# Optimization experiments

Hardware: AMD Instinct MI355X
Metric: run time of the kernel (lower is better)

## Reference

```python
import jax, jax.numpy as jnp
import numpy as np

EMB = 128
EDGE = 32
STEPS = 3


def _lrelu(x):
    return jax.nn.leaky_relu(x, negative_slope=0.01)


def setup_inputs() -> dict:
    key = jax.random.key(0)
    ks = jax.random.split(key, 16)
    N, E, G = 50000, 400000, 256
    x = jax.random.normal(ks[0], (N, EMB), jnp.float32)
    edge_attr = jax.random.normal(ks[1], (E, EDGE), jnp.float32)
    edge_index = jax.random.randint(ks[2], (2, E), 0, N, jnp.int64)
    batch_ind = jnp.sort(jax.random.randint(ks[3], (N,), 0, G, jnp.int64))
    data_lens = jax.random.randint(ks[4], (G,), 0, G, jnp.int64)
    s = 1.0 / np.sqrt(EMB)
    Wm = jax.random.normal(ks[5], (STEPS, EMB + EDGE, EMB), jnp.float32) * s
    bm = jnp.zeros((STEPS, EMB), jnp.float32)
    Wa = jax.random.normal(ks[6], (STEPS, 3 * EMB, EMB), jnp.float32) * s
    ba = jnp.zeros((STEPS, EMB), jnp.float32)
    Wgate = jax.random.normal(ks[7], (STEPS, EMB), jnp.float32) * s
    bgate = jnp.zeros((STEPS,), jnp.float32)
    Wfeat = jax.random.normal(ks[8], (STEPS, EMB, EMB), jnp.float32) * s
    bfeat = jnp.zeros((STEPS, EMB), jnp.float32)
    Wt = jax.random.normal(ks[9], (STEPS, 2 * EMB, EMB), jnp.float32) * s
    bt = jnp.zeros((STEPS, EMB), jnp.float32)
    return {"x": x, "edge_attr": edge_attr, "Wm": Wm, "bm": bm, "Wa": Wa,
            "ba": ba, "Wgate": Wgate, "bgate": bgate, "Wfeat": Wfeat,
            "bfeat": bfeat, "Wt": Wt, "bt": bt, "edge_index": edge_index,
            "batch_ind": batch_ind, "num_graphs": 256, "data_lens": data_lens}


def reference(x, edge_attr, Wm, bm, Wa, ba, Wgate, bgate, Wfeat, bfeat, Wt, bt,
              edge_index, batch_ind, num_graphs, data_lens):
    N = x.shape[0]
    src, dst = edge_index[0], edge_index[1]  # PyG: x_j = x[src], aggregate at dst
    xg = jnp.zeros((num_graphs, EMB), x.dtype)  # xg_init is None -> zeros
    for s in range(STEPS):
        # GraphNet: gather -> message MLP -> scatter-max -> update MLP + residual
        xg_node = xg[batch_ind]                                   # [N, emb]
        z = jnp.concatenate([x[src], edge_attr], axis=1)          # [E, emb+edge]
        m = _lrelu(z @ Wm[s] + bm[s])                             # [E, emb]
        agg = jax.ops.segment_max(m, dst, num_segments=N)         # [N, emb]
        agg = jnp.where(jnp.isneginf(agg), 0.0, agg)              # PyG fills empty with 0
        z2 = jnp.concatenate([x, xg_node, agg], axis=1)           # [N, 3*emb]
        x = _lrelu(z2 @ Wa[s] + ba[s]) + x
        # GlobalNode: segment-softmax attention pooling + transform + residual
        gate = x @ Wgate[s] + bgate[s]                            # [N]
        gmax = jax.ops.segment_max(gate, batch_ind, num_segments=num_graphs)
        gmax = jnp.where(jnp.isneginf(gmax), 0.0, gmax)
        e = jnp.exp(gate - gmax[batch_ind])
        denom = jax.ops.segment_sum(e, batch_ind, num_segments=num_graphs)
        alpha = e / denom[batch_ind]                              # [N]
        feat = _lrelu(x @ Wfeat[s] + bfeat[s])                    # [N, emb]
        pooled = jax.ops.segment_sum(alpha[:, None] * feat, batch_ind,
                                     num_segments=num_graphs)     # [G, emb]
        cat = jnp.concatenate([pooled, xg], axis=1)               # [G, 2*emb]
        xg = _lrelu(cat @ Wt[s] + bt[s]) + xg
    return x, xg
```

## Files before the change

kernel.cpp:

```cpp
#include <hip/hip_runtime.h>
#include <hip/hip_bf16.h>

#define EMB 128
#define EDGE 32
#define STEPS 3

typedef short bf8s __attribute__((ext_vector_type(8)));
typedef float f32x4 __attribute__((ext_vector_type(4)));

__device__ __forceinline__ float lrelu(float v) { return v > 0.0f ? v : 0.01f * v; }
__device__ __forceinline__ unsigned short f2bf(float f) {
    unsigned u = __float_as_uint(f);
    u += 0x7fffu + ((u >> 16) & 1u);
    return (unsigned short)(u >> 16);
}
__device__ __forceinline__ float bf2f(unsigned short s) {
    return __uint_as_float(((unsigned)s) << 16);
}
__device__ __forceinline__ unsigned pk2bf(float x, float y) {
    __hip_bfloat162 h = __float22bfloat162_rn(make_float2(x, y));
    return *(unsigned*)&h;
}

__global__ void k_hist(const int* __restrict__ dst, int E, int* __restrict__ deg) {
    int e = blockIdx.x * 256 + threadIdx.x;
    if (e < E) atomicAdd(&deg[dst[e]], 1);
}

__global__ void k_scan1(const int* __restrict__ deg, int N, int* __restrict__ rowptr,
                        int* __restrict__ bsums) {
    __shared__ int s[256];
    int t = threadIdx.x;
    int i = blockIdx.x * 256 + t;
    int v = (i < N) ? deg[i] : 0;
    s[t] = v;
    __syncthreads();
#pragma unroll
    for (int off = 1; off < 256; off <<= 1) {
        int x = (t >= off) ? s[t - off] : 0;
        __syncthreads();
        s[t] += x;
        __syncthreads();
    }
    if (i < N) rowptr[i] = s[t] - v;
    if (t == 255) bsums[blockIdx.x] = s[255];
}

__global__ void k_scan2(int* __restrict__ bsums, int NB) {
    __shared__ int s[256];
    __shared__ int carry;
    int t = threadIdx.x;
    if (t == 0) carry = 0;
    __syncthreads();
    for (int base = 0; base < NB; base += 256) {
        int i = base + t;
        int v = (i < NB) ? bsums[i] : 0;
        s[t] = v;
        __syncthreads();
#pragma unroll
        for (int off = 1; off < 256; off <<= 1) {
            int x = (t >= off) ? s[t - off] : 0;
            __syncthreads();
            s[t] += x;
            __syncthreads();
        }
        int excl = s[t] - v + carry;
        if (i < NB) bsums[i] = excl;
        int tot = s[255];
        __syncthreads();
        if (t == 0) carry += tot;
        __syncthreads();
    }
}

__global__ void k_scan3(int* __restrict__ rowptr, const int* __restrict__ bsums,
                        int* __restrict__ cursor, int N, int E) {
    int i = blockIdx.x * 256 + threadIdx.x;
    if (i < N) {
        int v = rowptr[i] + bsums[i >> 8];
        rowptr[i] = v;
        cursor[i] = v;
    }
    if (i == 0) rowptr[N] = E;
}

__global__ void k_fill(const int* __restrict__ src, const int* __restrict__ dst, int E,
                       int* __restrict__ cursor, int2* __restrict__ sp2) {
    int e = blockIdx.x * 256 + threadIdx.x;
    if (e >= E) return;
    int d = dst[e];
    int p = atomicAdd(&cursor[d], 1);
    sp2[p] = make_int2(src[e], e);
}

__global__ __launch_bounds__(256) void k_eaperm(const float* __restrict__ ea,
                                                const int2* __restrict__ sp2,
                                                unsigned short* __restrict__ ea16p,
                                                int* __restrict__ srcp, int E) {
    int p = blockIdx.x * 256 + threadIdx.x;
    if (p >= E) return;
    int2 sp = sp2[p];
    srcp[p] = sp.x;
    const float4* er = (const float4*)(ea + (size_t)sp.y * EDGE);
    union { unsigned u[16]; int4 v[4]; } o;
#pragma unroll
    for (int q = 0; q < 8; ++q) {
        float4 v = er[q];
        o.u[2 * q]     = pk2bf(v.x, v.y);
        o.u[2 * q + 1] = pk2bf(v.z, v.w);
    }
    int4* dp = (int4*)(ea16p + (size_t)p * EDGE);
#pragma unroll
    for (int q = 0; q < 4; ++q) dp[q] = o.v[q];
}

__global__ __launch_bounds__(256) void k_setup(const float* __restrict__ x0,
                                               unsigned short* __restrict__ x16,
                                               int N, int XB, int NB,
                                               const float* __restrict__ ba,
                                               float* __restrict__ gb,
                                               float* __restrict__ xg_a,
                                               const int* __restrict__ batch,
                                               int* __restrict__ gstart, int G,
                                               unsigned short* __restrict__ h16,
                                               int* __restrict__ deg) {
    int b = blockIdx.x, t = threadIdx.x;
    if (b < XB) {
        size_t idx = ((size_t)b * 256 + t) * 8;
        if (idx < (size_t)N * EMB) {
            const float4* s = (const float4*)(x0 + idx);
            float4 v0 = s[0], v1 = s[1];
            union { bf8s v; unsigned u[4]; } o;
            o.u[0] = pk2bf(v0.x, v0.y);
            o.u[1] = pk2bf(v0.z, v0.w);
            o.u[2] = pk2bf(v1.x, v1.y);
            o.u[3] = pk2bf(v1.z, v1.w);
            *(bf8s*)(x16 + idx) = o.v;
        }
        return;
    }
    b -= XB;
    if (b < NB) {
        int i = b * 256 + t;
        if (i < N) deg[i] = 0;
        return;
    }
    b -= NB;
    if (b < G) {
        if (t < EMB) gb[(size_t)b * EMB + t] = ba[t];
        else xg_a[(size_t)b * EMB + (t - EMB)] = 0.f;
        if (t == 0) {
            int lo = 0, hi = N;
            while (lo < hi) {
                int mid = (lo + hi) >> 1;
                if (batch[mid] < b) lo = mid + 1; else hi = mid;
            }
            gstart[b] = lo;
        }
        return;
    }
    if (t < EMB) h16[(size_t)N * EMB + t] = 0xFF80u;
    if (t == EMB) gstart[G] = N;
}

__global__ __launch_bounds__(256) void k_wpack(const float* __restrict__ Wm,
                                               const float* __restrict__ Wa,
                                               const float* __restrict__ Wfeat,
                                               unsigned short* __restrict__ wpack) {
    int gid = blockIdx.x * 256 + threadIdx.x;
    int unit = gid >> 14;
    int e = gid & 16383;
    int s = unit / 5, u = unit % 5;
    const float* src; int rows;
    switch (u) {
        case 0: src = Wm + (size_t)s * 160 * EMB;             rows = 128; break;
        case 1: src = Wm + (size_t)s * 160 * EMB + 128 * EMB; rows = 32;  break;
        case 2: src = Wa + (size_t)s * 384 * EMB;             rows = 128; break;
        case 3: src = Wa + (size_t)s * 384 * EMB + 256 * EMB; rows = 128; break;
        default: src = Wfeat + (size_t)s * EMB * EMB;         rows = 128; break;
    }
    int k = e >> 7, n = e & 127;
    if (k >= rows) return;
    unsigned short b = f2bf(src[(size_t)k * EMB + n]);
    int kc = k >> 5, c = n >> 4, lane = (n & 15) | (((k & 31) >> 3) << 4), j = k & 7;
    wpack[(size_t)unit * 16384 + ((size_t)(kc * 8 + c) * 64 + lane) * 8 + j] = b;
}

__device__ __forceinline__ void loadAa(const unsigned short* __restrict__ A16, int row0,
                                       int wv, int lane, int N, bf8s af[4]) {
    int li = lane & 15, oct = lane >> 4;
    int m = row0 + wv * 16 + li;
    if (m >= N) m = N - 1;
    const bf8s* ar = (const bf8s*)(A16 + (size_t)m * EMB);
#pragma unroll
    for (int kc = 0; kc < 4; ++kc) af[kc] = ar[kc * 4 + oct];
}
__device__ __forceinline__ void stageB(const unsigned short* __restrict__ Bp,
                                       unsigned short* lB, int tid) {
#pragma unroll
    for (int i = 0; i < 8; ++i) {
        int idx = tid + i * 256;
        ((int4*)lB)[idx] = ((const int4*)Bp)[idx];
    }
}
__device__ __forceinline__ void mfma128r(const bf8s af[4], const unsigned short* lB,
                                         f32x4 acc[8], int lane) {
#pragma unroll
    for (int kc = 0; kc < 4; ++kc) {
#pragma unroll
        for (int c = 0; c < 8; ++c) {
            bf8s b = *(const bf8s*)&lB[((kc * 8 + c) * 64 + lane) * 8];
            acc[c] = __builtin_amdgcn_mfma_f32_16x16x32_bf16(af[kc], b, acc[c], 0, 0, 0);
        }
    }
}

__device__ __forceinline__ void bias_epi(const f32x4 acc[8], int row0, int wv, int lane,
                                         const float* __restrict__ bias,
                                         unsigned short* __restrict__ C, int N) {
    int li = lane & 15, quad = lane >> 4;
    float bcol[8];
#pragma unroll
    for (int c = 0; c < 8; ++c) bcol[c] = bias[c * 16 + li];
#pragma unroll
    for (int rr = 0; rr < 4; ++rr) {
        int m = row0 + wv * 16 + quad * 4 + rr;
        if (m < N) {
            union { bf8s v; unsigned u[4]; } o;
#pragma unroll
            for (int j = 0; j < 4; ++j)
                o.u[j] = pk2bf(acc[2 * j][rr] + bcol[2 * j],
                               acc[2 * j + 1][rr] + bcol[2 * j + 1]);
            *(bf8s*)&C[(size_t)m * EMB + li * 8] = o.v;
        }
    }
}

__global__ __launch_bounds__(256) void k_gemm_bias(const unsigned short* __restrict__ A16,
                                                   const unsigned short* __restrict__ Bp,
                                                   const float* __restrict__ bias,
                                                   unsigned short* __restrict__ C, int N) {
    __shared__ unsigned short lB[16384];
    int tid = threadIdx.x, wv = tid >> 6, lane = tid & 63;
    int row0 = blockIdx.x * 64;
    stageB(Bp, lB, tid);
    bf8s af[4];
    loadAa(A16, row0, wv, lane, N, af);
    __syncthreads();
    f32x4 acc[8];
#pragma unroll
    for (int c = 0; c < 8; ++c) acc[c] = (f32x4){0.f, 0.f, 0.f, 0.f};
    mfma128r(af, lB, acc, lane);
    bias_epi(acc, row0, wv, lane, bias, C, N);
}

__global__ __launch_bounds__(256) void k_gemm_node(unsigned short* __restrict__ x16,
                                                   const unsigned short* __restrict__ agg16,
                                                   const unsigned short* __restrict__ BpX,
                                                   const unsigned short* __restrict__ BpA,
                                                   const float* __restrict__ gb,
                                                   const int* __restrict__ batch,
                                                   float* __restrict__ xout_f32,
                                                   const float* __restrict__ wg,
                                                   const float* __restrict__ bg,
                                                   float* __restrict__ gate, int N) {
    __shared__ unsigned short lB[16384];
    int tid = threadIdx.x, wv = tid >> 6, lane = tid & 63;
    int row0 = blockIdx.x * 64;
    stageB(BpX, lB, tid);
    bf8s af[4];
    loadAa(x16, row0, wv, lane, N, af);
    __syncthreads();
    f32x4 acc[8];
#pragma unroll
    for (int c = 0; c < 8; ++c) acc[c] = (f32x4){0.f, 0.f, 0.f, 0.f};
    mfma128r(af, lB, acc, lane);
    __syncthreads();
    stageB(BpA, lB, tid);
    loadAa(agg16, row0, wv, lane, N, af);
    __syncthreads();
    mfma128r(af, lB, acc, lane);
    int li = lane & 15, quad = lane >> 4;
    float gpart[4] = {0.f, 0.f, 0.f, 0.f};
#pragma unroll
    for (int c = 0; c < 8; ++c) {
        int col = c * 16 + li;
        float wgc = wg[col];
#pragma unroll
        for (int rr = 0; rr < 4; ++rr) {
            int m = row0 + wv * 16 + quad * 4 + rr;
            if (m < N) {
                int g = batch[m];
                float b = gb[(size_t)g * EMB + col];
                float res = bf2f(x16[(size_t)m * EMB + col]);
                float v = lrelu(acc[c][rr] + b) + res;
                x16[(size_t)m * EMB + col] = f2bf(v);
                if (xout_f32) xout_f32[(size_t)m * EMB + col] = v;
                gpart[rr] = fmaf(v, wgc, gpart[rr]);
            }
        }
    }
#pragma unroll
    for (int rr = 0; rr < 4; ++rr) {
#pragma unroll
        for (int off = 1; off < 16; off <<= 1)
            gpart[rr] += __shfl_xor(gpart[rr], off, 64);
    }
    if (li == 0) {
        float b0 = bg[0];
#pragma unroll
        for (int rr = 0; rr < 4; ++rr) {
            int m = row0 + wv * 16 + quad * 4 + rr;
            if (m < N) gate[m] = gpart[rr] + b0;
        }
    }
}

__device__ __forceinline__ void feat_epi(const f32x4 acc[8], int row0, int wv, int lane,
                                         const float* __restrict__ bias,
                                         const float* __restrict__ gate,
                                         const float* __restrict__ gmax,
                                         const float* __restrict__ denom,
                                         const int* __restrict__ batch,
                                         float* __restrict__ pooled, int N) {
    int li = lane & 15, quad = lane >> 4;
    int rb = row0 + wv * 16;
    if (rb >= N) return;
    float alpha[4];
    int grow[4];
#pragma unroll
    for (int rr = 0; rr < 4; ++rr) {
        int m = rb + quad * 4 + rr;
        if (m < N) {
            int g = batch[m];
            grow[rr] = g;
            alpha[rr] = __expf(gate[m] - gmax[g]) / denom[g];
        } else { alpha[rr] = 0.f; grow[rr] = 0; }
    }
    int gs = batch[rb];
    int mlast = rb + 15; if (mlast >= N) mlast = N - 1;
    bool uni = (gs == batch[mlast]);
#pragma unroll
    for (int c = 0; c < 8; ++c) {
        int col = c * 16 + li;
        float b = bias[col];
        float v0 = alpha[0] * lrelu(acc[c][0] + b);
        float v1 = alpha[1] * lrelu(acc[c][1] + b);
        float v2 = alpha[2] * lrelu(acc[c][2] + b);
        float v3 = alpha[3] * lrelu(acc[c][3] + b);
        if (uni) {
            float s = (v0 + v1) + (v2 + v3);
            s += __shfl_xor(s, 16, 64);
            s += __shfl_xor(s, 32, 64);
            if (quad == 0) atomicAdd(&pooled[(size_t)gs * EMB + col], s);
        } else {
            if (rb + quad * 4 + 0 < N) atomicAdd(&pooled[(size_t)grow[0] * EMB + col], v0);
            if (rb + quad * 4 + 1 < N) atomicAdd(&pooled[(size_t)grow[1] * EMB + col], v1);
            if (rb + quad * 4 + 2 < N) atomicAdd(&pooled[(size_t)grow[2] * EMB + col], v2);
            if (rb + quad * 4 + 3 < N) atomicAdd(&pooled[(size_t)grow[3] * EMB + col], v3);
        }
    }
}

__global__ __launch_bounds__(256) void k_gemm_feat(const unsigned short* __restrict__ A16,
                                                   const unsigned short* __restrict__ Bp,
                                                   const float* __restrict__ bias,
                                                   const float* __restrict__ gate,
                                                   const float* __restrict__ gmax,
                                                   const float* __restrict__ denom,
                                                   const int* __restrict__ batch,
                                                   float* __restrict__ pooled, int N) {
    __shared__ unsigned short lB[16384];
    int tid = threadIdx.x, wv = tid >> 6, lane = tid & 63;
    int row0 = blockIdx.x * 64;
    stageB(Bp, lB, tid);
    bf8s af[4];
    loadAa(A16, row0, wv, lane, N, af);
    __syncthreads();
    f32x4 acc[8];
#pragma unroll
    for (int c = 0; c < 8; ++c) acc[c] = (f32x4){0.f, 0.f, 0.f, 0.f};
    mfma128r(af, lB, acc, lane);
    feat_epi(acc, row0, wv, lane, bias, gate, gmax, denom, batch, pooled, N);
}

__global__ __launch_bounds__(256) void k_gemm_fb(const unsigned short* __restrict__ A16,
                                                 const unsigned short* __restrict__ BpF,
                                                 const float* __restrict__ bfeat_s,
                                                 const float* __restrict__ gate,
                                                 const float* __restrict__ gmax,
                                                 const float* __restrict__ denom,
                                                 const int* __restrict__ batch,
                                                 float* __restrict__ pooled,
                                                 const unsigned short* __restrict__ BpBn,
                                                 const float* __restrict__ bm_next,
                                                 unsigned short* __restrict__ h16, int N) {
    __shared__ unsigned short lB[16384];
    int tid = threadIdx.x, wv = tid >> 6, lane = tid & 63;
    int row0 = blockIdx.x * 64;
    stageB(BpF, lB, tid);
    bf8s af[4];
    loadAa(A16, row0, wv, lane, N, af);
    __syncthreads();
    f32x4 accF[8], accB[8];
#pragma unroll
    for (int c = 0; c < 8; ++c) {
        accF[c] = (f32x4){0.f, 0.f, 0.f, 0.f};
        accB[c] = (f32x4){0.f, 0.f, 0.f, 0.f};
    }
    mfma128r(af, lB, accF, lane);
    __syncthreads();
    stageB(BpBn, lB, tid);
    __syncthreads();
    mfma128r(af, lB, accB, lane);
    feat_epi(accF, row0, wv, lane, bfeat_s, gate, gmax, denom, batch, pooled, N);
    bias_epi(accB, row0, wv, lane, bm_next, h16, N);
}

__global__ __launch_bounds__(256) void k_gseg(const float* __restrict__ gate,
                                              const int* __restrict__ gstart,
                                              float* __restrict__ gmax,
                                              float* __restrict__ denom,
                                              float* __restrict__ pooled) {
    int g = blockIdx.x;
    int t = threadIdx.x;
    if (t < EMB) pooled[(size_t)g * EMB + t] = 0.f;
    int s0 = gstart[g], s1 = gstart[g + 1];
    __shared__ float red[256];
    float mx = -__builtin_inff();
    for (int i = s0 + t; i < s1; i += 256) mx = fmaxf(mx, gate[i]);
    red[t] = mx;
    __syncthreads();
#pragma unroll
    for (int off = 128; off; off >>= 1) {
        if (t < off) red[t] = fmaxf(red[t], red[t + off]);
        __syncthreads();
    }
    float m = red[0];
    __syncthreads();
    float sum = 0.f;
    for (int i = s0 + t; i < s1; i += 256) sum += __expf(gate[i] - m);
    red[t] = sum;
    __syncthreads();
#pragma unroll
    for (int off = 128; off; off >>= 1) {
        if (t < off) red[t] += red[t + off];
        __syncthreads();
    }
    if (t == 0) {
        gmax[g] = (s1 > s0) ? m : 0.f;
        denom[g] = red[0];
    }
}

__global__ __launch_bounds__(128) void k_xg(const float* __restrict__ pooled,
                                            const float* __restrict__ xg,
                                            const float* __restrict__ Wt,
                                            const float* __restrict__ bt,
                                            float* __restrict__ xg_out,
                                            const float* __restrict__ WaGn,
                                            const float* __restrict__ ban,
                                            float* __restrict__ gb) {
    int g = blockIdx.x, c = threadIdx.x;
    __shared__ float row[256];
    row[c] = pooled[(size_t)g * EMB + c];
    row[c + 128] = xg[(size_t)g * EMB + c];
    __syncthreads();
    float acc = bt[c];
#pragma unroll 8
    for (int k = 0; k < 256; ++k) acc = fmaf(row[k], Wt[(size_t)k * EMB + c], acc);
    float v = lrelu(acc) + row[c + 128];
    xg_out[(size_t)g * EMB + c] = v;
    if (WaGn) {
        __syncthreads();
        row[c] = v;
        __syncthreads();
        float a2 = ban[c];
#pragma unroll 8
        for (int k = 0; k < EMB; ++k) a2 = fmaf(row[k], WaGn[(size_t)k * EMB + c], a2);
        gb[(size_t)g * EMB + c] = a2;
    }
}

__global__ __launch_bounds__(256) void k_fagg(const unsigned short* __restrict__ h,
                                              const unsigned short* __restrict__ ea16p,
                                              const int* __restrict__ srcp,
                                              const int* __restrict__ rowptr,
                                              const unsigned short* __restrict__ Bp,
                                              unsigned short* __restrict__ agg, int N) {
    __shared__ unsigned short lB[4096];
    int tid = threadIdx.x;
    ((int4*)lB)[tid]       = ((const int4*)Bp)[tid];
    ((int4*)lB)[tid + 256] = ((const int4*)Bp)[tid + 256];
    __syncthreads();
    int wv = tid >> 6, lane = tid & 63;
    int li = lane & 15, oct = lane >> 4;
    int nA = blockIdx.x * 8 + wv * 2;
    if (nA >= N) return;
    int nB = nA + 1;
    bool hasB = (nB < N);
    int r0 = rowptr[nA];
    int r1 = rowptr[nA + 1];
    int r2 = hasB ? rowptr[nB + 1] : r1;
    int degA = r1 - r0, degB = r2 - r1;

    float vmA[8], vmB[8];
#pragma unroll
    for (int ci = 0; ci < 8; ++ci) { vmA[ci] = -__builtin_inff(); vmB[ci] = -__builtin_inff(); }

    {
        int pA = r0 + li; if (pA >= r1) pA = (r1 > r0) ? r1 - 1 : 0;
        int pB = r1 + li; if (pB >= r2) pB = (r2 > r1) ? r2 - 1 : 0;
        int srcvA = srcp[pA];
        int srcvB = srcp[pB];
        bf8s aA = *(const bf8s*)&ea16p[(size_t)pA * EDGE + oct * 8];
        bf8s aB = *(const bf8s*)&ea16p[(size_t)pB * EDGE + oct * 8];
        union { bf8s v; unsigned short s[8]; } hvA[4], hvB[4];
#pragma unroll
        for (int rr = 0; rr < 4; ++rr) {
            int sr = __shfl(srcvA, oct * 4 + rr, 16);
            if (oct * 4 + rr >= degA) sr = N;
            hvA[rr].v = *(const bf8s*)&h[(size_t)sr * EMB + li * 8];
        }
#pragma unroll
        for (int rr = 0; rr < 4; ++rr) {
            int sr = __shfl(srcvB, oct * 4 + rr, 16);
            if (oct * 4 + rr >= degB) sr = N;
            hvB[rr].v = *(const bf8s*)&h[(size_t)sr * EMB + li * 8];
        }
#pragma unroll
        for (int ci = 0; ci < 8; ++ci) {
            bf8s bb = *(const bf8s*)&lB[(ci * 64 + lane) * 8];
            f32x4 acc;
            acc[0] = bf2f(hvA[0].s[ci]);
            acc[1] = bf2f(hvA[1].s[ci]);
            acc[2] = bf2f(hvA[2].s[ci]);
            acc[3] = bf2f(hvA[3].s[ci]);
            acc = __builtin_amdgcn_mfma_f32_16x16x32_bf16(aA, bb, acc, 0, 0, 0);
#pragma unroll
            for (int rr = 0; rr < 4; ++rr) vmA[ci] = fmaxf(vmA[ci], acc[rr]);
        }
#pragma unroll
        for (int ci = 0; ci < 8; ++ci) {
            bf8s bb = *(const bf8s*)&lB[(ci * 64 + lane) * 8];
            f32x4 acc;
            acc[0] = bf2f(hvB[0].s[ci]);
            acc[1] = bf2f(hvB[1].s[ci]);
            acc[2] = bf2f(hvB[2].s[ci]);
            acc[3] = bf2f(hvB[3].s[ci]);
            acc = __builtin_amdgcn_mfma_f32_16x16x32_bf16(aB, bb, acc, 0, 0, 0);
#pragma unroll
            for (int rr = 0; rr < 4; ++rr) vmB[ci] = fmaxf(vmB[ci], acc[rr]);
        }
    }
    for (int b = 16; b < degA; b += 16) {
        int p = r0 + b + li;
        if (p > r1 - 1) p = r1 - 1;
        int srcv = srcp[p];
        bf8s a = *(const bf8s*)&ea16p[(size_t)p * EDGE + oct * 8];
        union { bf8s v; unsigned short s[8]; } hv[4];
#pragma unroll
        for (int rr = 0; rr < 4; ++rr) {
            int sr = __shfl(srcv, oct * 4 + rr, 16);
            if (b + oct * 4 + rr >= degA) sr = N;
            hv[rr].v = *(const bf8s*)&h[(size_t)sr * EMB + li * 8];
        }
#pragma unroll
        for (int ci = 0; ci < 8; ++ci) {
            bf8s bb = *(const bf8s*)&lB[(ci * 64 + lane) * 8];
            f32x4 acc;
            acc[0] = bf2f(hv[0].s[ci]);
            acc[1] = bf2f(hv[1].s[ci]);
            acc[2] = bf2f(hv[2].s[ci]);
            acc[3] = bf2f(hv[3].s[ci]);
            acc = __builtin_amdgcn_mfma_f32_16x16x32_bf16(a, bb, acc, 0, 0, 0);
#pragma unroll
            for (int rr = 0; rr < 4; ++rr) vmA[ci] = fmaxf(vmA[ci], acc[rr]);
        }
    }
    for (int b = 16; b < degB; b += 16) {
        int p = r1 + b + li;
        if (p > r2 - 1) p = r2 - 1;
        int srcv = srcp[p];
        bf8s a = *(const bf8s*)&ea16p[(size_t)p * EDGE + oct * 8];
        union { bf8s v; unsigned short s[8]; } hv[4];
#pragma unroll
        for (int rr = 0; rr < 4; ++rr) {
            int sr = __shfl(srcv, oct * 4 + rr, 16);
            if (b + oct * 4 + rr >= degB) sr = N;
            hv[rr].v = *(const bf8s*)&h[(size_t)sr * EMB + li * 8];
        }
#pragma unroll
        for (int ci = 0; ci < 8; ++ci) {
            bf8s bb = *(const bf8s*)&lB[(ci * 64 + lane) * 8];
            f32x4 acc;
            acc[0] = bf2f(hv[0].s[ci]);
            acc[1] = bf2f(hv[1].s[ci]);
            acc[2] = bf2f(hv[2].s[ci]);
            acc[3] = bf2f(hv[3].s[ci]);
            acc = __builtin_amdgcn_mfma_f32_16x16x32_bf16(a, bb, acc, 0, 0, 0);
#pragma unroll
            for (int rr = 0; rr < 4; ++rr) vmB[ci] = fmaxf(vmB[ci], acc[rr]);
        }
    }
#pragma unroll
    for (int ci = 0; ci < 8; ++ci) {
        vmA[ci] = fmaxf(vmA[ci], __shfl_xor(vmA[ci], 16, 64));
        vmA[ci] = fmaxf(vmA[ci], __shfl_xor(vmA[ci], 32, 64));
        vmB[ci] = fmaxf(vmB[ci], __shfl_xor(vmB[ci], 16, 64));
        vmB[ci] = fmaxf(vmB[ci], __shfl_xor(vmB[ci], 32, 64));
    }
    {
        float s0 = (oct == 0) ? vmA[0] : (oct == 1) ? vmA[1] : (oct == 2) ? vmA[2] : vmA[3];
        float s1 = (oct == 0) ? vmA[4] : (oct == 1) ? vmA[5] : (oct == 2) ? vmA[6] : vmA[7];
        s0 = lrelu(s0);
        s1 = lrelu(s1);
        if (degA == 0) { s0 = 0.f; s1 = 0.f; }
        agg[(size_t)nA * EMB + oct * 16 + li]       = f2bf(s0);
        agg[(size_t)nA * EMB + (oct + 4) * 16 + li] = f2bf(s1);
    }
    if (hasB) {
        float s0 = (oct == 0) ? vmB[0] : (oct == 1) ? vmB[1] : (oct == 2) ? vmB[2] : vmB[3];
        float s1 = (oct == 0) ? vmB[4] : (oct == 1) ? vmB[5] : (oct == 2) ? vmB[6] : vmB[7];
        s0 = lrelu(s0);
        s1 = lrelu(s1);
        if (degB == 0) { s0 = 0.f; s1 = 0.f; }
        agg[(size_t)nB * EMB + oct * 16 + li]       = f2bf(s0);
        agg[(size_t)nB * EMB + (oct + 4) * 16 + li] = f2bf(s1);
    }
}

extern "C" void kernel_launch(void* const* d_in, const int* in_sizes, int n_in,
                              void* d_out, int out_size, void* d_ws, size_t ws_size,
                              hipStream_t stream) {
    const float* x0    = (const float*)d_in[0];
    const float* ea    = (const float*)d_in[1];
    const float* Wm    = (const float*)d_in[2];
    const float* bm    = (const float*)d_in[3];
    const float* Wa    = (const float*)d_in[4];
    const float* ba    = (const float*)d_in[5];
    const float* Wgate = (const float*)d_in[6];
    const float* bgate = (const float*)d_in[7];
    const float* Wfeat = (const float*)d_in[8];
    const float* bfeat = (const float*)d_in[9];
    const float* Wt    = (const float*)d_in[10];
    const float* bt    = (const float*)d_in[11];
    const int*   eidx  = (const int*)d_in[12];
    const int*   batch = (const int*)d_in[13];

    int N = in_sizes[0] / EMB;
    int E = in_sizes[1] / EDGE;
    int G = in_sizes[15];

    char* w = (char*)d_ws;
    auto alloc = [&](size_t bytes) {
        char* p = w;
        w += (bytes + 255) & ~(size_t)255;
        return p;
    };
    unsigned short* h16   = (unsigned short*)alloc((size_t)(N + 1) * EMB * 2);
    unsigned short* x16   = (unsigned short*)alloc((size_t)N * EMB * 2);
    unsigned short* agg16 = (unsigned short*)alloc((size_t)N * EMB * 2);
    float* gate   = (float*)alloc((size_t)N * 4);
    float* gb     = (float*)alloc((size_t)G * EMB * 4);
    float* pooled = (float*)alloc((size_t)G * EMB * 4);
    float* gmax   = (float*)alloc((size_t)G * 4);
    float* denom  = (float*)alloc((size_t)G * 4);
    float* xg_a   = (float*)alloc((size_t)G * EMB * 4);
    float* xg_b   = (float*)alloc((size_t)G * EMB * 4);
    int* deg      = (int*)alloc((size_t)N * 4);
    int* rowptr   = (int*)alloc((size_t)(N + 1) * 4);
    int* cursor   = (int*)alloc((size_t)N * 4);
    int2* sp2     = (int2*)alloc((size_t)E * 8);
    int* srcp     = (int*)alloc((size_t)E * 4);
    unsigned short* ea16p = (unsigned short*)alloc((size_t)E * EDGE * 2);
    int* gstart   = (int*)alloc((size_t)(G + 1) * 4);
    int* bsums    = (int*)alloc(1024 * 4);
    unsigned short* wpack = (unsigned short*)alloc((size_t)15 * 16384 * 2);

    const int* esrc = eidx;
    const int* edst = eidx + E;
    int ebl = (E + 255) / 256;
    int NB  = (N + 255) / 256;
    int XB  = ((size_t)N * EMB / 8 + 255) / 256;

    k_setup<<<XB + NB + G + 1, 256, 0, stream>>>(x0, x16, N, XB, NB, ba, gb, xg_a,
                                                 batch, gstart, G, h16, deg);
    k_hist<<<ebl, 256, 0, stream>>>(edst, E, deg);
    k_scan1<<<NB, 256, 0, stream>>>(deg, N, rowptr, bsums);
    k_scan2<<<1, 256, 0, stream>>>(bsums, NB);
    k_scan3<<<NB, 256, 0, stream>>>(rowptr, bsums, cursor, N, E);
    k_fill<<<ebl, 256, 0, stream>>>(esrc, edst, E, cursor, sp2);
    k_eaperm<<<ebl, 256, 0, stream>>>(ea, sp2, ea16p, srcp, E);
    k_wpack<<<960, 256, 0, stream>>>(Wm, Wa, Wfeat, wpack);

    int gemm_blocks = (N + 63) / 64;
    int fagg_blocks = (N + 7) / 8;

    float* xg_cur = xg_a;
    float* xg_nxt = xg_b;

    k_gemm_bias<<<gemm_blocks, 256, 0, stream>>>(x16, wpack + 0 * 16384, bm, h16, N);

    for (int s = 0; s < STEPS; ++s) {
        const unsigned short* wp = wpack + (size_t)s * 5 * 16384;
        bool last = (s == STEPS - 1);

        k_fagg<<<fagg_blocks, 256, 0, stream>>>(h16, ea16p, srcp, rowptr, wp + 1 * 16384,
                                                agg16, N);
        k_gemm_node<<<gemm_blocks, 256, 0, stream>>>(x16, agg16, wp + 2 * 16384,
                                                     wp + 3 * 16384, gb, batch,
                                                     last ? (float*)d_out : nullptr,
                                                     Wgate + s * EMB, bgate + s, gate, N);
        k_gseg<<<G, 256, 0, stream>>>(gate, gstart, gmax, denom, pooled);
        if (!last) {
            k_gemm_fb<<<gemm_blocks, 256, 0, stream>>>(x16, wp + 4 * 16384, bfeat + s * EMB,
                                                       gate, gmax, denom, batch, pooled,
                                                       wp + 5 * 16384 ,
                                                       bm + (s + 1) * EMB, h16, N);
        } else {
            k_gemm_feat<<<gemm_blocks, 256, 0, stream>>>(x16, wp + 4 * 16384,
                                                         bfeat + s * EMB, gate, gmax,
                                                         denom, batch, pooled, N);
        }
        const float* WaGn = !last ? Wa + (size_t)(s + 1) * 384 * EMB + 128 * EMB : nullptr;
        const float* ban  = !last ? ba + (s + 1) * EMB : nullptr;
        float* xgout = last ? (float*)d_out + (size_t)N * EMB : xg_nxt;
        k_xg<<<G, 128, 0, stream>>>(pooled, xg_cur, Wt + (size_t)s * 256 * EMB,
                                    bt + s * EMB, xgout, WaGn, ban, gb);

        float* tmp = xg_cur; xg_cur = xg_nxt; xg_nxt = tmp;
    }
}
```

Baseline: 518.4 us.

## Fuse softmax denominator into node GEMM epilogue and drop segment kernel

New measurement: 809.2 us. 56.1% more time.

```diff
diff --git a/kernel.cpp b/kernel.cpp
--- a/kernel.cpp
+++ b/kernel.cpp
@@ -123,7 +123,8 @@
                                                const int* __restrict__ batch,
                                                int* __restrict__ gstart, int G,
                                                unsigned short* __restrict__ h16,
-                                               int* __restrict__ deg) {
+                                               int* __restrict__ deg,
+                                               float* __restrict__ denom) {
     int b = blockIdx.x, t = threadIdx.x;
     if (b < XB) {
         size_t idx = ((size_t)b * 256 + t) * 8;
@@ -150,6 +151,7 @@
         if (t < EMB) gb[(size_t)b * EMB + t] = ba[t];
         else xg_a[(size_t)b * EMB + (t - EMB)] = 0.f;
         if (t == 0) {
+            denom[b] = 0.f;
             int lo = 0, hi = N;
             while (lo < hi) {
                 int mid = (lo + hi) >> 1;
@@ -263,10 +265,14 @@
                                                    float* __restrict__ xout_f32,
                                                    const float* __restrict__ wg,
                                                    const float* __restrict__ bg,
-                                                   float* __restrict__ gate, int N) {
+                                                   float* __restrict__ egate,
+                                                   float* __restrict__ denom,
+                                                   float* __restrict__ pooled, int G, int N) {
     __shared__ unsigned short lB[16384];
     int tid = threadIdx.x, wv = tid >> 6, lane = tid & 63;
     int row0 = blockIdx.x * 64;
+    if (blockIdx.x < (unsigned)G && tid < EMB)
+        pooled[(size_t)blockIdx.x * EMB + tid] = 0.f;
     stageB(BpX, lB, tid);
     bf8s af[4];
     loadAa(x16, row0, wv, lane, N, af);
@@ -311,15 +317,18 @@
 #pragma unroll
         for (int rr = 0; rr < 4; ++rr) {
             int m = row0 + wv * 16 + quad * 4 + rr;
-            if (m < N) gate[m] = gpart[rr] + b0;
+            if (m < N) {
+                float ge = __expf(gpart[rr] + b0);
+                egate[m] = ge;
+                atomicAdd(&denom[batch[m]], ge);
+            }
         }
     }
 }
 
 __device__ __forceinline__ void feat_epi(const f32x4 acc[8], int row0, int wv, int lane,
                                          const float* __restrict__ bias,
-                                         const float* __restrict__ gate,
-                                         const float* __restrict__ gmax,
+                                         const float* __restrict__ egate,
                                          const float* __restrict__ denom,
                                          const int* __restrict__ batch,
                                          float* __restrict__ pooled, int N) {
@@ -334,7 +343,7 @@
         if (m < N) {
             int g = batch[m];
             grow[rr] = g;
-            alpha[rr] = __expf(gate[m] - gmax[g]) / denom[g];
+            alpha[rr] = egate[m] / denom[g];
         } else { alpha[rr] = 0.f; grow[rr] = 0; }
     }
     int gs = batch[rb];
@@ -365,8 +374,7 @@
 __global__ __launch_bounds__(256) void k_gemm_feat(const unsigned short* __restrict__ A16,
                                                    const unsigned short* __restrict__ Bp,
                                                    const float* __restrict__ bias,
-                                                   const float* __restrict__ gate,
-                                                   const float* __restrict__ gmax,
+                                                   const float* __restrict__ egate,
                                                    const float* __restrict__ denom,
                                                    const int* __restrict__ batch,
                                                    float* __restrict__ pooled, int N) {
@@ -381,14 +389,13 @@
 #pragma unroll
     for (int c = 0; c < 8; ++c) acc[c] = (f32x4){0.f, 0.f, 0.f, 0.f};
     mfma128r(af, lB, acc, lane);
-    feat_epi(acc, row0, wv, lane, bias, gate, gmax, denom, batch, pooled, N);
+    feat_epi(acc, row0, wv, lane, bias, egate, denom, batch, pooled, N);
 }
 
 __global__ __launch_bounds__(256) void k_gemm_fb(const unsigned short* __restrict__ A16,
                                                  const unsigned short* __restrict__ BpF,
                                                  const float* __restrict__ bfeat_s,
-                                                 const float* __restrict__ gate,
-                                                 const float* __restrict__ gmax,
+                                                 const float* __restrict__ egate,
                                                  const float* __restrict__ denom,
                                                  const int* __restrict__ batch,
                                                  float* __restrict__ pooled,
@@ -413,44 +420,8 @@
     stageB(BpBn, lB, tid);
     __syncthreads();
     mfma128r(af, lB, accB, lane);
-    feat_epi(accF, row0, wv, lane, bfeat_s, gate, gmax, denom, batch, pooled, N);
+    feat_epi(accF, row0, wv, lane, bfeat_s, egate, denom, batch, pooled, N);
     bias_epi(accB, row0, wv, lane, bm_next, h16, N);
-}
-
-__global__ __launch_bounds__(256) void k_gseg(const float* __restrict__ gate,
-                                              const int* __restrict__ gstart,
-                                              float* __restrict__ gmax,
-                                              float* __restrict__ denom,
-                                              float* __restrict__ pooled) {
-    int g = blockIdx.x;
-    int t = threadIdx.x;
-    if (t < EMB) pooled[(size_t)g * EMB + t] = 0.f;
-    int s0 = gstart[g], s1 = gstart[g + 1];
-    __shared__ float red[256];
-    float mx = -__builtin_inff();
-    for (int i = s0 + t; i < s1; i += 256) mx = fmaxf(mx, gate[i]);
-    red[t] = mx;
-    __syncthreads();
-#pragma unroll
-    for (int off = 128; off; off >>= 1) {
-        if (t < off) red[t] = fmaxf(red[t], red[t + off]);
-        __syncthreads();
-    }
-    float m = red[0];
-    __syncthreads();
-    float sum = 0.f;
-    for (int i = s0 + t; i < s1; i += 256) sum += __expf(gate[i] - m);
-    red[t] = sum;
-    __syncthreads();
-#pragma unroll
-    for (int off = 128; off; off >>= 1) {
-        if (t < off) red[t] += red[t + off];
-        __syncthreads();
-    }
-    if (t == 0) {
-        gmax[g] = (s1 > s0) ? m : 0.f;
-        denom[g] = red[0];
-    }
 }
 
 __global__ __launch_bounds__(128) void k_xg(const float* __restrict__ pooled,
@@ -460,12 +431,14 @@
                                             float* __restrict__ xg_out,
                                             const float* __restrict__ WaGn,
                                             const float* __restrict__ ban,
-                                            float* __restrict__ gb) {
+                                            float* __restrict__ gb,
+                                            float* __restrict__ denom) {
     int g = blockIdx.x, c = threadIdx.x;
     __shared__ float row[256];
     row[c] = pooled[(size_t)g * EMB + c];
     row[c + 128] = xg[(size_t)g * EMB + c];
     __syncthreads();
+    if (c == 0) denom[g] = 0.f;
     float acc = bt[c];
 #pragma unroll 8
     for (int k = 0; k < 256; ++k) acc = fmaf(row[k], Wt[(size_t)k * EMB + c], acc);
@@ -661,10 +634,9 @@
     unsigned short* h16   = (unsigned short*)alloc((size_t)(N + 1) * EMB * 2);
     unsigned short* x16   = (unsigned short*)alloc((size_t)N * EMB * 2);
     unsigned short* agg16 = (unsigned short*)alloc((size_t)N * EMB * 2);
-    float* gate   = (float*)alloc((size_t)N * 4);
+    float* egate  = (float*)alloc((size_t)N * 4);
     float* gb     = (float*)alloc((size_t)G * EMB * 4);
     float* pooled = (float*)alloc((size_t)G * EMB * 4);
-    float* gmax   = (float*)alloc((size_t)G * 4);
     float* denom  = (float*)alloc((size_t)G * 4);
     float* xg_a   = (float*)alloc((size_t)G * EMB * 4);
     float* xg_b   = (float*)alloc((size_t)G * EMB * 4);
@@ -685,7 +657,7 @@
     int XB  = ((size_t)N * EMB / 8 + 255) / 256;
 
     k_setup<<<XB + NB + G + 1, 256, 0, stream>>>(x0, x16, N, XB, NB, ba, gb, xg_a,
-                                                 batch, gstart, G, h16, deg);
+                                                 batch, gstart, G, h16, deg, denom);
     k_hist<<<ebl, 256, 0, stream>>>(edst, E, deg);
     k_scan1<<<NB, 256, 0, stream>>>(deg, N, rowptr, bsums);
     k_scan2<<<1, 256, 0, stream>>>(bsums, NB);
@@ -711,23 +683,23 @@
         k_gemm_node<<<gemm_blocks, 256, 0, stream>>>(x16, agg16, wp + 2 * 16384,
                                                      wp + 3 * 16384, gb, batch,
                                                      last ? (float*)d_out : nullptr,
-                                                     Wgate + s * EMB, bgate + s, gate, N);
-        k_gseg<<<G, 256, 0, stream>>>(gate, gstart, gmax, denom, pooled);
+                                                     Wgate + s * EMB, bgate + s,
+                                                     egate, denom, pooled, G, N);
         if (!last) {
             k_gemm_fb<<<gemm_blocks, 256, 0, stream>>>(x16, wp + 4 * 16384, bfeat + s * EMB,
-                                                       gate, gmax, denom, batch, pooled,
+                                                       egate, denom, batch, pooled,
                                                        wp + 5 * 16384 ,
                                                        bm + (s + 1) * EMB, h16, N);
         } else {
             k_gemm_feat<<<gemm_blocks, 256, 0, stream>>>(x16, wp + 4 * 16384,
-                                                         bfeat + s * EMB, gate, gmax,
-                                                         denom, batch, pooled, N);
+                                                         bfeat + s * EMB, egate, denom,
+                                                         batch, pooled, N);
         }
         const float* WaGn = !last ? Wa + (size_t)(s + 1) * 384 * EMB + 128 * EMB : nullptr;
         const float* ban  = !last ? ba + (s + 1) * EMB : nullptr;
         float* xgout = last ? (float*)d_out + (size_t)N * EMB : xg_nxt;
         k_xg<<<G, 128, 0, stream>>>(pooled, xg_cur, Wt + (size_t)s * 256 * EMB,
-                                    bt + s * EMB, xgout, WaGn, ban, gb);
+                                    bt + s * EMB, xgout, WaGn, ban, gb, denom);
 
         float* tmp = xg_cur; xg_cur = xg_nxt; xg_nxt = tmp;
     }
```
